# Kernel optimization log

Hardware: AMD Instinct MI355X
Metric: run time of the kernel (lower is better)

## Reference

```python
import jax, jax.numpy as jnp
import numpy as np

T, B, INPUT_SIZE, NUM_NEURONS, OUTPUT_SIZE = 200, 256, 784, 1024, 10
TAU_M, V_REST, THRESH0, TAU_THRESH, BETA, DT = 20.0, -65.0, -50.0, 100.0, 5.0, 1.0


def setup_inputs() -> dict:
    key = jax.random.key(0)
    k1, k2, k3 = jax.random.split(key, 3)
    input_spikes = jax.random.uniform(k1, (T, B, INPUT_SIZE), dtype=jnp.float32)
    input_weights = jax.random.uniform(k2, (INPUT_SIZE, NUM_NEURONS), dtype=jnp.float32)
    # W_rec = -0.5 * (ones - eye): lateral inhibition buffer
    W_rec = -0.5 * (jnp.ones((NUM_NEURONS, NUM_NEURONS), jnp.float32) - jnp.eye(NUM_NEURONS, dtype=jnp.float32))
    output_weights = jax.random.uniform(k3, (NUM_NEURONS, OUTPUT_SIZE), dtype=jnp.float32)
    return {"input_spikes": input_spikes, "input_weights": input_weights,
            "W_rec": W_rec, "output_weights": output_weights}


def reference(input_spikes, input_weights, W_rec, output_weights):
    Bd = input_spikes.shape[1]
    n = input_weights.shape[1]
    mp0 = jnp.full((Bd, n), V_REST, jnp.float32)       # membrane potential
    th0 = jnp.full((Bd, n), THRESH0, jnp.float32)      # dynamic threshold
    h0 = jnp.zeros((Bd, n), jnp.float32)               # previous hidden spikes

    def step(carry, x_t):
        mp, th, prev = carry
        net = x_t @ input_weights + prev @ W_rec        # (B, n)
        mp = mp + (V_REST - mp) / TAU_M + net * DT
        spikes = (mp >= th).astype(jnp.float32)
        th = th + BETA * spikes - (th - THRESH0) / TAU_THRESH * DT
        mp = jnp.where(spikes > 0, V_REST, mp)          # reset on spike
        return (mp, th, spikes), spikes

    _, hidden_spikes = jax.lax.scan(step, (mp0, th0, h0), input_spikes)  # (T, B, n)
    spike_counts = hidden_spikes.sum(axis=0)            # (B, n)
    logits = spike_counts @ output_weights              # (B, out)
    return logits, hidden_spikes
```

## Files before the change

### kernel.cpp

```cpp
#include <hip/hip_runtime.h>


#define TT 200
#define BB 256
#define KK 784
#define NN 1024
#define OO 10

__global__ __launch_bounds__(256)
void gemm_net(const float* __restrict__ X, const float* __restrict__ W,
              float* __restrict__ C) {
  __shared__ float As[16][128];
  __shared__ float Bs[16][128];
  float4 (*As4)[32] = (float4(*)[32])As;
  float4 (*Bs4)[32] = (float4(*)[32])Bs;

  const int tid = threadIdx.x;
  const int n0 = blockIdx.x * 128;
  const int m0 = blockIdx.y * 128;
  const int tx = tid & 15;
  const int ty = tid >> 4;
  const int arow = tid >> 1;
  const int ak   = (tid & 1) * 8;
  const int brow = tid >> 5;
  const int bc   = (tid & 31) * 4;

  const float* ap = X + (size_t)(m0 + arow) * KK + ak;
  const float* bp = W + (size_t)brow * NN + n0 + bc;

  float4 a0 = *(const float4*)(ap);
  float4 a1 = *(const float4*)(ap + 4);
  float4 b0 = *(const float4*)(bp);
  float4 b1 = *(const float4*)(bp + 8 * NN);

  float acc[2][2][4][4] = {};

  for (int k0 = 0; k0 < KK; k0 += 16) {
    __syncthreads();
    As[ak + 0][arow] = a0.x;
    As[ak + 1][arow] = a0.y;
    As[ak + 2][arow] = a0.z;
    As[ak + 3][arow] = a0.w;
    As[ak + 4][arow] = a1.x;
    As[ak + 5][arow] = a1.y;
    As[ak + 6][arow] = a1.z;
    As[ak + 7][arow] = a1.w;
    *(float4*)&Bs[brow][bc] = b0;
    *(float4*)&Bs[brow + 8][bc] = b1;
    __syncthreads();

    if (k0 + 16 < KK) {
      ap += 16;
      bp += 16 * NN;
      a0 = *(const float4*)(ap);
      a1 = *(const float4*)(ap + 4);
      b0 = *(const float4*)(bp);
      b1 = *(const float4*)(bp + 8 * NN);
    }

#pragma unroll
    for (int k = 0; k < 16; ++k) {
      float4 A0 = As4[k][ty];
      float4 A1 = As4[k][16 + ty];
      float4 B0 = Bs4[k][tx];
      float4 B1 = Bs4[k][16 + tx];
      float av[2][4] = {{A0.x, A0.y, A0.z, A0.w}, {A1.x, A1.y, A1.z, A1.w}};
      float bv[2][4] = {{B0.x, B0.y, B0.z, B0.w}, {B1.x, B1.y, B1.z, B1.w}};
#pragma unroll
      for (int qi = 0; qi < 2; ++qi)
#pragma unroll
        for (int qj = 0; qj < 2; ++qj)
#pragma unroll
          for (int i = 0; i < 4; ++i)
#pragma unroll
            for (int j = 0; j < 4; ++j)
              acc[qi][qj][i][j] =
                  fmaf(av[qi][i], bv[qj][j], acc[qi][qj][i][j]);
    }
  }
#pragma unroll
  for (int qi = 0; qi < 2; ++qi)
#pragma unroll
    for (int i = 0; i < 4; ++i) {
      const int r = m0 + qi * 64 + ty * 4 + i;
#pragma unroll
      for (int qj = 0; qj < 2; ++qj) {
        float4 v = {acc[qi][qj][i][0], acc[qi][qj][i][1],
                    acc[qi][qj][i][2], acc[qi][qj][i][3]};
        *(float4*)(C + (size_t)r * NN + n0 + qj * 64 + tx * 4) = v;
      }
    }
}

__global__ __launch_bounds__(1024)
void snn_scan(float* __restrict__ hid, const float* __restrict__ Wout,
              float* __restrict__ logits) {
  constexpr float V_REST = -65.0f, THRESH0 = -50.0f, TAU_M = 20.0f,
                  TAU_TH = 100.0f, BETA = 5.0f, DT = 1.0f;
  const int b = blockIdx.x;
  const int tid = threadIdx.x;
  const int wave = tid >> 6, lane = tid & 63;
  __shared__ float s_part[2][16];
  __shared__ float s_log[16][OO];

  float mp = V_REST, th = THRESH0, prev = 0.0f, cnt = 0.0f;
  float S = 0.0f;
  const size_t base = (size_t)b * NN + tid;
  const size_t STEP = (size_t)BB * NN;

  float netc = hid[base];
  float netn = hid[STEP + base];

  for (int t = 0; t < TT; ++t) {
    float rec = -0.5f * (S - prev);
    float nv = netc + rec;
    float m = mp + (V_REST - mp) / TAU_M;
    m = m + nv * DT;
    bool spk = (m >= th);
    float s = spk ? 1.0f : 0.0f;
    th = (th + BETA * s) - ((th - THRESH0) / TAU_TH) * DT;
    mp = spk ? V_REST : m;
    cnt += s;
    prev = s;
    hid[(size_t)t * STEP + base] = s;

    float netf = 0.0f;
    if (t + 2 < TT) netf = hid[(size_t)(t + 2) * STEP + base];
    netc = netn;
    netn = netf;

    unsigned long long bal = __ballot(spk);
    if (lane == 0) s_part[t & 1][wave] = (float)__popcll(bal);
    __asm__ volatile("s_waitcnt lgkmcnt(0)\n\ts_barrier" ::: "memory");
    const float* sp = s_part[t & 1];
    float4 p0 = *(const float4*)(sp + 0);
    float4 p1 = *(const float4*)(sp + 4);
    float4 p2 = *(const float4*)(sp + 8);
    float4 p3 = *(const float4*)(sp + 12);
    S = ((p0.x + p0.y) + (p0.z + p0.w)) + ((p1.x + p1.y) + (p1.z + p1.w)) +
        ((p2.x + p2.y) + (p2.z + p2.w)) + ((p3.x + p3.y) + (p3.z + p3.w));
  }

  float lg[OO];
#pragma unroll
  for (int o = 0; o < OO; ++o) lg[o] = cnt * Wout[(size_t)tid * OO + o];
#pragma unroll
  for (int o = 0; o < OO; ++o) {
    float v = lg[o];
#pragma unroll
    for (int d = 32; d > 0; d >>= 1) v += __shfl_down(v, d, 64);
    if (lane == 0) s_log[wave][o] = v;
  }
  __syncthreads();
  if (tid < OO) {
    float v = 0.0f;
#pragma unroll
    for (int w = 0; w < 16; ++w) v += s_log[w][tid];
    logits[(size_t)b * OO + tid] = v;
  }
}

extern "C" void kernel_launch(void* const* d_in, const int* in_sizes, int n_in,
                              void* d_out, int out_size, void* d_ws,
                              size_t ws_size, hipStream_t stream) {
  const float* X    = (const float*)d_in[0];
  const float* Win  = (const float*)d_in[1];
  const float* Wout = (const float*)d_in[3];

  float* logits = (float*)d_out;
  float* hid    = (float*)d_out + BB * OO;

  dim3 g1(NN / 128, TT * BB / 128);
  gemm_net<<<g1, 256, 0, stream>>>(X, Win, hid);
  snn_scan<<<BB, 1024, 0, stream>>>(hid, Wout, logits);
}
```

Measured before the change: 1.316 ms.

## Double-buffer GEMM tiles via direct global-to-LDS loads with swizzled A layout

Replaces register-staged loads and transposed LDS stores in the input GEMM with global_load_lds direct-to-LDS copies into two ping-pong buffers. The A tile is now stored row-major with an XOR swizzle on 4-float chunks to avoid bank conflicts. The inner loop reads A as float4 along k instead of along m. This is meant to remove register round-trips and the scalar transposed LDS writes and to overlap loading the next tile with compute. It doubles LDS use and relies on loop-count arithmetic (K=784 is 49 tiles of 16) and on the direct-LDS builtin's per-wave addressing being correct.

```diff
diff --git a/kernel.cpp b/kernel.cpp
--- a/kernel.cpp
+++ b/kernel.cpp
@@ -7,77 +7,98 @@
 #define NN 1024
 #define OO 10
 
+__device__ __forceinline__ void gload_lds16(const float* g, float* l) {
+  __builtin_amdgcn_global_load_lds(
+      (const __attribute__((address_space(1))) void*)g,
+      (__attribute__((address_space(3))) void*)l, 16, 0, 0);
+}
+
+#define F4E(v, e) ((e) == 0 ? (v).x : (e) == 1 ? (v).y : (e) == 2 ? (v).z : (v).w)
+
 __global__ __launch_bounds__(256)
 void gemm_net(const float* __restrict__ X, const float* __restrict__ W,
               float* __restrict__ C) {
-  __shared__ float As[16][128];
-  __shared__ float Bs[16][128];
-  float4 (*As4)[32] = (float4(*)[32])As;
-  float4 (*Bs4)[32] = (float4(*)[32])Bs;
+  __shared__ float As[2][128][16];
+  __shared__ float Bs[2][16][128];
 
-  const int tid = threadIdx.x;
+  const int tid  = threadIdx.x;
+  const int lane = tid & 63;
+  const int w    = tid >> 6;
   const int n0 = blockIdx.x * 128;
   const int m0 = blockIdx.y * 128;
   const int tx = tid & 15;
   const int ty = tid >> 4;
-  const int arow = tid >> 1;
-  const int ak   = (tid & 1) * 8;
-  const int brow = tid >> 5;
-  const int bc   = (tid & 31) * 4;
+  const int tyq = ty & 3;
 
-  const float* ap = X + (size_t)(m0 + arow) * KK + ak;
-  const float* bp = W + (size_t)brow * NN + n0 + bc;
+  const int aR0 = w * 32 + (lane >> 2);
+  const int aCq = ((lane & 3) ^ ((lane >> 4) & 3)) * 4;
+  const float* aSrc0 = X + (size_t)(m0 + aR0) * KK + aCq;
+  const float* aSrc1 = X + (size_t)(m0 + aR0 + 16) * KK + aCq;
+  const int bR0 = w * 4 + (lane >> 5);
+  const int bCol = (lane & 31) * 4;
+  const float* bSrc0 = W + (size_t)bR0 * NN + n0 + bCol;
+  const float* bSrc1 = W + (size_t)(bR0 + 2) * NN + n0 + bCol;
 
-  float4 a0 = *(const float4*)(ap);
-  float4 a1 = *(const float4*)(ap + 4);
-  float4 b0 = *(const float4*)(bp);
-  float4 b1 = *(const float4*)(bp + 8 * NN);
+  const int wa = w * 32;
+  const int wb = w * 4;
+
+#define ISSUE(q)                                                          \
+  do {                                                                    \
+    gload_lds16(aSrc0, &As[q][wa][0]);                                    \
+    gload_lds16(aSrc1, &As[q][wa + 16][0]);                               \
+    gload_lds16(bSrc0, &Bs[q][wb][0]);                                    \
+    gload_lds16(bSrc1, &Bs[q][wb + 2][0]);                                \
+    aSrc0 += 16; aSrc1 += 16;                                             \
+    bSrc0 += 16 * NN; bSrc1 += 16 * NN;                                   \
+  } while (0)
 
   float acc[2][2][4][4] = {};
 
-  for (int k0 = 0; k0 < KK; k0 += 16) {
+#define COMPUTE(q)                                                        \
+  do {                                                                    \
+    _Pragma("unroll") for (int kq = 0; kq < 4; ++kq) {                    \
+      float4 bq[4][2];                                                    \
+      _Pragma("unroll") for (int dk = 0; dk < 4; ++dk) {                  \
+        bq[dk][0] = *(const float4*)&Bs[q][kq * 4 + dk][tx * 4];          \
+        bq[dk][1] = *(const float4*)&Bs[q][kq * 4 + dk][64 + tx * 4];     \
+      }                                                                   \
+      _Pragma("unroll") for (int qi = 0; qi < 2; ++qi) {                  \
+        _Pragma("unroll") for (int i = 0; i < 4; ++i) {                   \
+          const int m = qi * 64 + ty * 4 + i;                             \
+          float4 a4 = *(const float4*)&As[q][m][(kq ^ tyq) * 4];          \
+          _Pragma("unroll") for (int dk = 0; dk < 4; ++dk) {              \
+            _Pragma("unroll") for (int qj = 0; qj < 2; ++qj) {            \
+              acc[qi][qj][i][0] =                                         \
+                  fmaf(F4E(a4, dk), bq[dk][qj].x, acc[qi][qj][i][0]);     \
+              acc[qi][qj][i][1] =                                         \
+                  fmaf(F4E(a4, dk), bq[dk][qj].y, acc[qi][qj][i][1]);     \
+              acc[qi][qj][i][2] =                                         \
+                  fmaf(F4E(a4, dk), bq[dk][qj].z, acc[qi][qj][i][2]);     \
+              acc[qi][qj][i][3] =                                         \
+                  fmaf(F4E(a4, dk), bq[dk][qj].w, acc[qi][qj][i][3]);     \
+            }                                                             \
+          }                                                               \
+        }                                                                 \
+      }                                                                   \
+    }                                                                     \
+  } while (0)
+
+  ISSUE(0);
+  __syncthreads();
+
+  for (int p = 0; p < 24; ++p) {
+    ISSUE(1);
+    COMPUTE(0);
     __syncthreads();
-    As[ak + 0][arow] = a0.x;
-    As[ak + 1][arow] = a0.y;
-    As[ak + 2][arow] = a0.z;
-    As[ak + 3][arow] = a0.w;
-    As[ak + 4][arow] = a1.x;
-    As[ak + 5][arow] = a1.y;
-    As[ak + 6][arow] = a1.z;
-    As[ak + 7][arow] = a1.w;
-    *(float4*)&Bs[brow][bc] = b0;
-    *(float4*)&Bs[brow + 8][bc] = b1;
+    ISSUE(0);
+    COMPUTE(1);
     __syncthreads();
+  }
+  COMPUTE(0);
 
-    if (k0 + 16 < KK) {
-      ap += 16;
-      bp += 16 * NN;
-      a0 = *(const float4*)(ap);
-      a1 = *(const float4*)(ap + 4);
-      b0 = *(const float4*)(bp);
-      b1 = *(const float4*)(bp + 8 * NN);
-    }
+#undef ISSUE
+#undef COMPUTE
 
-#pragma unroll
-    for (int k = 0; k < 16; ++k) {
-      float4 A0 = As4[k][ty];
-      float4 A1 = As4[k][16 + ty];
-      float4 B0 = Bs4[k][tx];
-      float4 B1 = Bs4[k][16 + tx];
-      float av[2][4] = {{A0.x, A0.y, A0.z, A0.w}, {A1.x, A1.y, A1.z, A1.w}};
-      float bv[2][4] = {{B0.x, B0.y, B0.z, B0.w}, {B1.x, B1.y, B1.z, B1.w}};
-#pragma unroll
-      for (int qi = 0; qi < 2; ++qi)
-#pragma unroll
-        for (int qj = 0; qj < 2; ++qj)
-#pragma unroll
-          for (int i = 0; i < 4; ++i)
-#pragma unroll
-            for (int j = 0; j < 4; ++j)
-              acc[qi][qj][i][j] =
-                  fmaf(av[qi][i], bv[qj][j], acc[qi][qj][i][j]);
-    }
-  }
 #pragma unroll
   for (int qi = 0; qi < 2; ++qi)
 #pragma unroll
```

New measurement: 1.592 ms. +21.0%, slower.

## Halve scan block size with two neurons per thread; swap GEMM grid order

Applied to the files above, without the earlier changes.

The scan kernel now launches 512 threads per batch row, and each thread handles two neurons. This halves the number of waves that join each per-timestep barrier and lets the two neurons' updates and loads overlap. Separately, the GEMM grid is transposed so consecutive blocks walk along M rather than N, which changes L2 reuse of the weight and input tiles. The cost is more work per thread and possibly lower latency hiding in the scan.

```diff
diff --git a/kernel.cpp b/kernel.cpp
--- a/kernel.cpp
+++ b/kernel.cpp
@@ -16,8 +16,8 @@
   float4 (*Bs4)[32] = (float4(*)[32])Bs;
 
   const int tid = threadIdx.x;
-  const int n0 = blockIdx.x * 128;
-  const int m0 = blockIdx.y * 128;
+  const int m0 = blockIdx.x * 128;
+  const int n0 = blockIdx.y * 128;
   const int tx = tid & 15;
   const int ty = tid >> 4;
   const int arow = tid >> 1;
@@ -92,7 +92,7 @@
     }
 }
 
-__global__ __launch_bounds__(1024)
+__global__ __launch_bounds__(512)
 void snn_scan(float* __restrict__ hid, const float* __restrict__ Wout,
               float* __restrict__ logits) {
   constexpr float V_REST = -65.0f, THRESH0 = -50.0f, TAU_M = 20.0f,
@@ -100,50 +100,68 @@
   const int b = blockIdx.x;
   const int tid = threadIdx.x;
   const int wave = tid >> 6, lane = tid & 63;
-  __shared__ float s_part[2][16];
-  __shared__ float s_log[16][OO];
+  __shared__ float s_part[2][8];
+  __shared__ float s_log[8][OO];
 
-  float mp = V_REST, th = THRESH0, prev = 0.0f, cnt = 0.0f;
+  float mpA = V_REST, thA = THRESH0, prevA = 0.0f, cntA = 0.0f;
+  float mpB = V_REST, thB = THRESH0, prevB = 0.0f, cntB = 0.0f;
   float S = 0.0f;
-  const size_t base = (size_t)b * NN + tid;
+  const size_t baseA = (size_t)b * NN + tid;
+  const size_t baseB = baseA + 512;
   const size_t STEP = (size_t)BB * NN;
 
-  float netc = hid[base];
-  float netn = hid[STEP + base];
+  float cA = hid[baseA], cB = hid[baseB];
+  float nA = hid[STEP + baseA], nB = hid[STEP + baseB];
 
   for (int t = 0; t < TT; ++t) {
-    float rec = -0.5f * (S - prev);
-    float nv = netc + rec;
-    float m = mp + (V_REST - mp) / TAU_M;
-    m = m + nv * DT;
-    bool spk = (m >= th);
-    float s = spk ? 1.0f : 0.0f;
-    th = (th + BETA * s) - ((th - THRESH0) / TAU_TH) * DT;
-    mp = spk ? V_REST : m;
-    cnt += s;
-    prev = s;
-    hid[(size_t)t * STEP + base] = s;
+    float recA = -0.5f * (S - prevA);
+    float nvA = cA + recA;
+    float mA = mpA + (V_REST - mpA) / TAU_M;
+    mA = mA + nvA * DT;
+    bool sA = (mA >= thA);
+    float fA = sA ? 1.0f : 0.0f;
+    thA = (thA + BETA * fA) - ((thA - THRESH0) / TAU_TH) * DT;
+    mpA = sA ? V_REST : mA;
+    cntA += fA;
+    prevA = fA;
+    float recB = -0.5f * (S - prevB);
+    float nvB = cB + recB;
+    float mB = mpB + (V_REST - mpB) / TAU_M;
+    mB = mB + nvB * DT;
+    bool sB = (mB >= thB);
+    float fB = sB ? 1.0f : 0.0f;
+    thB = (thB + BETA * fB) - ((thB - THRESH0) / TAU_TH) * DT;
+    mpB = sB ? V_REST : mB;
+    cntB += fB;
+    prevB = fB;
 
-    float netf = 0.0f;
-    if (t + 2 < TT) netf = hid[(size_t)(t + 2) * STEP + base];
-    netc = netn;
-    netn = netf;
+    hid[(size_t)t * STEP + baseA] = fA;
+    hid[(size_t)t * STEP + baseB] = fB;
 
-    unsigned long long bal = __ballot(spk);
-    if (lane == 0) s_part[t & 1][wave] = (float)__popcll(bal);
+    float fAn = 0.0f, fBn = 0.0f;
+    if (t + 2 < TT) {
+      fAn = hid[(size_t)(t + 2) * STEP + baseA];
+      fBn = hid[(size_t)(t + 2) * STEP + baseB];
+    }
+    cA = nA; nA = fAn;
+    cB = nB; nB = fBn;
+
+    unsigned long long balA = __ballot(sA);
+    unsigned long long balB = __ballot(sB);
+    if (lane == 0)
+      s_part[t & 1][wave] = (float)(__popcll(balA) + __popcll(balB));
     __asm__ volatile("s_waitcnt lgkmcnt(0)\n\ts_barrier" ::: "memory");
     const float* sp = s_part[t & 1];
     float4 p0 = *(const float4*)(sp + 0);
     float4 p1 = *(const float4*)(sp + 4);
-    float4 p2 = *(const float4*)(sp + 8);
-    float4 p3 = *(const float4*)(sp + 12);
-    S = ((p0.x + p0.y) + (p0.z + p0.w)) + ((p1.x + p1.y) + (p1.z + p1.w)) +
-        ((p2.x + p2.y) + (p2.z + p2.w)) + ((p3.x + p3.y) + (p3.z + p3.w));
+    S = ((p0.x + p0.y) + (p0.z + p0.w)) + ((p1.x + p1.y) + (p1.z + p1.w));
   }
 
   float lg[OO];
 #pragma unroll
-  for (int o = 0; o < OO; ++o) lg[o] = cnt * Wout[(size_t)tid * OO + o];
+  for (int o = 0; o < OO; ++o)
+    lg[o] = cntA * Wout[(size_t)tid * OO + o] +
+            cntB * Wout[(size_t)(tid + 512) * OO + o];
 #pragma unroll
   for (int o = 0; o < OO; ++o) {
     float v = lg[o];
@@ -155,7 +173,7 @@
   if (tid < OO) {
     float v = 0.0f;
 #pragma unroll
-    for (int w = 0; w < 16; ++w) v += s_log[w][tid];
+    for (int w = 0; w < 8; ++w) v += s_log[w][tid];
     logits[(size_t)b * OO + tid] = v;
   }
 }
@@ -170,7 +188,7 @@
   float* logits = (float*)d_out;
   float* hid    = (float*)d_out + BB * OO;
 
-  dim3 g1(NN / 128, TT * BB / 128);
+  dim3 g1(TT * BB / 128, NN / 128);
   gemm_net<<<g1, 256, 0, stream>>>(X, Win, hid);
-  snn_scan<<<BB, 1024, 0, stream>>>(hid, Wout, logits);
+  snn_scan<<<BB, 512, 0, stream>>>(hid, Wout, logits);
 }
```

Result: faster. 1.236 ms (-6.1%).

## Run SNN scan in a single wavefront per batch row, removing block barriers

Applied to the files above, without the earlier changes.

The scan kernel now uses one 64-lane wavefront per batch row. Each lane owns 16 neurons in registers and computes the population spike count with ballot/popcount, so the per-timestep LDS write and block barrier are gone. The time loop is unrolled by two with double-buffered float4 prefetch of the net input. The GEMM grid axes are also swapped so consecutive blocks walk along M. The trade-off is 256 single-wave blocks with a longer serial dependency chain per lane, which lowers occupancy and latency hiding.

```diff
diff --git a/kernel.cpp b/kernel.cpp
--- a/kernel.cpp
+++ b/kernel.cpp
@@ -16,8 +16,8 @@
   float4 (*Bs4)[32] = (float4(*)[32])Bs;
 
   const int tid = threadIdx.x;
-  const int n0 = blockIdx.x * 128;
-  const int m0 = blockIdx.y * 128;
+  const int m0 = blockIdx.x * 128;
+  const int n0 = blockIdx.y * 128;
   const int tx = tid & 15;
   const int ty = tid >> 4;
   const int arow = tid >> 1;
@@ -92,71 +92,92 @@
     }
 }
 
-__global__ __launch_bounds__(1024)
+#define F4SET(v, e, val)                                                   \
+  ((e) == 0 ? ((v).x = (val))                                              \
+            : (e) == 1 ? ((v).y = (val))                                   \
+                       : (e) == 2 ? ((v).z = (val)) : ((v).w = (val)))
+#define F4GET(v, e) ((e) == 0 ? (v).x : (e) == 1 ? (v).y : (e) == 2 ? (v).z : (v).w)
+
+__global__ __launch_bounds__(64)
 void snn_scan(float* __restrict__ hid, const float* __restrict__ Wout,
               float* __restrict__ logits) {
   constexpr float V_REST = -65.0f, THRESH0 = -50.0f, TAU_M = 20.0f,
                   TAU_TH = 100.0f, BETA = 5.0f, DT = 1.0f;
   const int b = blockIdx.x;
-  const int tid = threadIdx.x;
-  const int wave = tid >> 6, lane = tid & 63;
-  __shared__ float s_part[2][16];
-  __shared__ float s_log[16][OO];
-
-  float mp = V_REST, th = THRESH0, prev = 0.0f, cnt = 0.0f;
-  float S = 0.0f;
-  const size_t base = (size_t)b * NN + tid;
+  const int lane = threadIdx.x;
+  const size_t rowbase = (size_t)b * NN + (size_t)lane * 4;
   const size_t STEP = (size_t)BB * NN;
 
-  float netc = hid[base];
-  float netn = hid[STEP + base];
+  float mp[16], th[16], prev[16], cnt[16];
+#pragma unroll
+  for (int u = 0; u < 16; ++u) {
+    mp[u] = V_REST; th[u] = THRESH0; prev[u] = 0.0f; cnt[u] = 0.0f;
+  }
+  float S = 0.0f;
 
-  for (int t = 0; t < TT; ++t) {
-    float rec = -0.5f * (S - prev);
-    float nv = netc + rec;
-    float m = mp + (V_REST - mp) / TAU_M;
-    m = m + nv * DT;
-    bool spk = (m >= th);
-    float s = spk ? 1.0f : 0.0f;
-    th = (th + BETA * s) - ((th - THRESH0) / TAU_TH) * DT;
-    mp = spk ? V_REST : m;
-    cnt += s;
-    prev = s;
-    hid[(size_t)t * STEP + base] = s;
+  float4 p0[4], p1[4];
+#pragma unroll
+  for (int c = 0; c < 4; ++c) {
+    p0[c] = *(const float4*)&hid[rowbase + c * 256];
+    p1[c] = *(const float4*)&hid[STEP + rowbase + c * 256];
+  }
 
-    float netf = 0.0f;
-    if (t + 2 < TT) netf = hid[(size_t)(t + 2) * STEP + base];
-    netc = netn;
-    netn = netf;
+#define SCAN_STEP(t, P)                                                    \
+  do {                                                                     \
+    int Si = 0;                                                            \
+    _Pragma("unroll") for (int c = 0; c < 4; ++c) {                        \
+      float4 f4;                                                           \
+      _Pragma("unroll") for (int e = 0; e < 4; ++e) {                      \
+        const int u = c * 4 + e;                                           \
+        float net = F4GET(P[c], e);                                        \
+        float rec = -0.5f * (S - prev[u]);                                 \
+        float nv = net + rec;                                              \
+        float m = mp[u] + (V_REST - mp[u]) / TAU_M;                        \
+        m = m + nv * DT;                                                   \
+        bool sp = (m >= th[u]);                                            \
+        float f = sp ? 1.0f : 0.0f;                                        \
+        th[u] = (th[u] + BETA * f) - ((th[u] - THRESH0) / TAU_TH) * DT;    \
+        mp[u] = sp ? V_REST : m;                                           \
+        cnt[u] += f;                                                       \
+        prev[u] = f;                                                       \
+        Si += __popcll(__ballot(sp));                                      \
+        F4SET(f4, e, f);                                                   \
+      }                                                                    \
+      *(float4*)&hid[(size_t)(t) * STEP + rowbase + c * 256] = f4;         \
+    }                                                                      \
+    if ((t) + 2 < TT) {                                                    \
+      _Pragma("unroll") for (int c = 0; c < 4; ++c)                        \
+        P[c] = *(const float4*)&hid[(size_t)((t) + 2) * STEP + rowbase +   \
+                                    c * 256];                              \
+    }                                                                      \
+    S = (float)Si;                                                         \
+  } while (0)
 
-    unsigned long long bal = __ballot(spk);
-    if (lane == 0) s_part[t & 1][wave] = (float)__popcll(bal);
-    __asm__ volatile("s_waitcnt lgkmcnt(0)\n\ts_barrier" ::: "memory");
-    const float* sp = s_part[t & 1];
-    float4 p0 = *(const float4*)(sp + 0);
-    float4 p1 = *(const float4*)(sp + 4);
-    float4 p2 = *(const float4*)(sp + 8);
-    float4 p3 = *(const float4*)(sp + 12);
-    S = ((p0.x + p0.y) + (p0.z + p0.w)) + ((p1.x + p1.y) + (p1.z + p1.w)) +
-        ((p2.x + p2.y) + (p2.z + p2.w)) + ((p3.x + p3.y) + (p3.z + p3.w));
+  for (int t = 0; t < TT; t += 2) {
+    SCAN_STEP(t + 0, p0);
+    SCAN_STEP(t + 1, p1);
   }
+#undef SCAN_STEP
 
   float lg[OO];
 #pragma unroll
-  for (int o = 0; o < OO; ++o) lg[o] = cnt * Wout[(size_t)tid * OO + o];
+  for (int o = 0; o < OO; ++o) lg[o] = 0.0f;
+#pragma unroll
+  for (int c = 0; c < 4; ++c)
+#pragma unroll
+    for (int e = 0; e < 4; ++e) {
+      const int u = c * 4 + e;
+      const int j = c * 256 + lane * 4 + e;
+#pragma unroll
+      for (int o = 0; o < OO; ++o)
+        lg[o] = fmaf(cnt[u], Wout[(size_t)j * OO + o], lg[o]);
+    }
 #pragma unroll
   for (int o = 0; o < OO; ++o) {
     float v = lg[o];
 #pragma unroll
     for (int d = 32; d > 0; d >>= 1) v += __shfl_down(v, d, 64);
-    if (lane == 0) s_log[wave][o] = v;
-  }
-  __syncthreads();
-  if (tid < OO) {
-    float v = 0.0f;
-#pragma unroll
-    for (int w = 0; w < 16; ++w) v += s_log[w][tid];
-    logits[(size_t)b * OO + tid] = v;
+    if (lane == 0) logits[(size_t)b * OO + o] = v;
   }
 }
 
@@ -170,7 +191,7 @@
   float* logits = (float*)d_out;
   float* hid    = (float*)d_out + BB * OO;
 
-  dim3 g1(NN / 128, TT * BB / 128);
+  dim3 g1(TT * BB / 128, NN / 128);
   gemm_net<<<g1, 256, 0, stream>>>(X, Win, hid);
-  snn_scan<<<BB, 1024, 0, stream>>>(hid, Wout, logits);
+  snn_scan<<<BB, 64, 0, stream>>>(hid, Wout, logits);
 }
```

Result: no change. 1.309 ms (-0.5%).
